# Kernel tuning notes

Hardware: AMD Instinct MI355X
Metric: run time of the kernel (lower is better)

Reference implementation:

```python
import jax, jax.numpy as jnp
import numpy as np

BATCH = 2
SEQ = 2048
D_MODEL = 512
D_STATE = 16
D_CONV = 4
D_INNER = 2 * D_MODEL  # expand=2


def setup_inputs() -> dict:
    key = jax.random.key(0)
    ks = jax.random.split(key, 7)
    s = 0.02
    x = jax.random.normal(ks[0], (BATCH, SEQ, D_MODEL), jnp.float32)
    W_in = jax.random.normal(ks[1], (2 * D_INNER, D_MODEL), jnp.float32) * s
    conv_w = jax.random.normal(ks[2], (D_INNER, 1, D_CONV), jnp.float32) * s  # depthwise kernel
    conv_b = jnp.zeros((D_INNER,), jnp.float32)
    W_x = jax.random.normal(ks[3], (2 * D_STATE, D_INNER), jnp.float32) * s
    W_dt = jax.random.normal(ks[4], (D_INNER, D_INNER), jnp.float32) * s
    b_dt = jnp.zeros((D_INNER,), jnp.float32)
    # A_log init: log of [1..d_state] broadcast over d_inner rows
    A_log = jnp.log(jnp.broadcast_to(jnp.arange(1, D_STATE + 1, dtype=jnp.float32), (D_INNER, D_STATE)))
    D_param = jnp.ones((D_INNER,), jnp.float32)
    W_out = jax.random.normal(ks[5], (D_MODEL, D_INNER), jnp.float32) * s
    return dict(x=x, W_in=W_in, conv_w=conv_w, conv_b=conv_b, W_x=W_x,
                W_dt=W_dt, b_dt=b_dt, A_log=A_log, D_param=D_param, W_out=W_out)


def reference(x, W_in, conv_w, conv_b, W_x, W_dt, b_dt, A_log, D_param, W_out):
    # in_proj, split into x-branch and gate z
    xz = x @ W_in.T                             # [B, L, 2*di]
    xi, z = jnp.split(xz, 2, axis=-1)
    # depthwise causal conv1d (torch pads both sides then slices [:seq_len] == left-pad only)
    h = jnp.transpose(xi, (0, 2, 1))            # [B, di, L]
    h = jax.lax.conv_general_dilated(
        h, conv_w, window_strides=(1,), padding=[(D_CONV - 1, 0)],
        dimension_numbers=('NCH', 'OIH', 'NCH'), feature_group_count=D_INNER)
    h = h + conv_b[None, :, None]
    h = jax.nn.silu(jnp.transpose(h, (0, 2, 1)))  # [B, L, di]

    A = -jnp.exp(A_log)                         # [di, ds]
    x_dbl = h @ W_x.T                           # [B, L, 2*ds]
    _delta_unused, Bmat = jnp.split(x_dbl, 2, axis=-1)  # B (also used as C): [B, L, ds]
    delta = jax.nn.softplus(h @ W_dt.T + b_dt)  # [B, L, di] (overwrites x_proj delta, as in source)

    def step(state, inp):
        d_t, B_t, h_t = inp                     # [B,di], [B,ds], [B,di]
        dA = jnp.exp(d_t[:, :, None] * A)       # [B, di, ds]
        state = dA * state + d_t[:, :, None] * B_t[:, None, :] * h_t[:, :, None]
        y_t = jnp.einsum('bds,bs->bd', state, B_t)  # C == B
        return state, y_t

    init = jnp.zeros((x.shape[0], D_INNER, D_STATE), x.dtype)
    _, ys = jax.lax.scan(step, init,
                         (jnp.swapaxes(delta, 0, 1), jnp.swapaxes(Bmat, 0, 1), jnp.swapaxes(h, 0, 1)))
    y = jnp.swapaxes(ys, 0, 1)                  # [B, L, di]
    y = (y + D_param * h) * jax.nn.silu(z)
    return y @ W_out.T                          # [B, L, d_model]
```

## Files before the change

### kernel.cpp

```cpp
#include <hip/hip_runtime.h>
#include <cstddef>
#include <cstdint>

#define NB 2
#define L_SEQ 2048
#define DM 512
#define DS 16
#define DI 1024
#define NC 64
#define CL (L_SEQ/NC)

typedef __attribute__((ext_vector_type(4))) float f32x4;
typedef __attribute__((ext_vector_type(8))) short bf16x8;

__device__ __forceinline__ float softplus_f(float x) {
  return (x > 20.f) ? x : log1pf(expf(x));
}
__device__ __forceinline__ float silu_f(float x) {
  return x / (1.f + expf(-x));
}
__device__ __forceinline__ ushort f2bf(float f) {
  uint32_t u = __float_as_uint(f);
  return (ushort)((u + 0x7fffu + ((u >> 16) & 1u)) >> 16);
}
__device__ __forceinline__ float bf2f(ushort h) {
  return __uint_as_float(((uint32_t)h) << 16);
}

__device__ __forceinline__ void gload16(const void* g, ushort* lds_wave_base) {
  __builtin_amdgcn_global_load_lds(
      (const __attribute__((address_space(1))) void*)g,
      (__attribute__((address_space(3))) void*)lds_wave_base, 16, 0, 0);
}

template <int N>
__device__ __forceinline__ void wait_vm() {
  if constexpr (N == 0)      asm volatile("s_waitcnt vmcnt(0)" ::: "memory");
  else if constexpr (N == 4) asm volatile("s_waitcnt vmcnt(4)" ::: "memory");
  else if constexpr (N == 6) asm volatile("s_waitcnt vmcnt(6)" ::: "memory");
  else if constexpr (N == 8) asm volatile("s_waitcnt vmcnt(8)" ::: "memory");
}

__global__ __launch_bounds__(256) void split_bf16(
    const float* __restrict__ in, ushort* __restrict__ hi,
    ushort* __restrict__ lo, int n4) {
  int i = blockIdx.x * 256 + threadIdx.x;
  if (i >= n4) return;
  float4 v = ((const float4*)in)[i];
  ushort h0 = f2bf(v.x), h1 = f2bf(v.y), h2 = f2bf(v.z), h3 = f2bf(v.w);
  ((ushort4*)hi)[i] = make_ushort4(h0, h1, h2, h3);
  ((ushort4*)lo)[i] = make_ushort4(
      f2bf(v.x - bf2f(h0)), f2bf(v.y - bf2f(h1)),
      f2bf(v.z - bf2f(h2)), f2bf(v.w - bf2f(h3)));
}

template <int BM, int BN, int ACT>
__global__ __launch_bounds__(256) void gemm_mfma(
    const ushort* __restrict__ Ahi, const ushort* __restrict__ Alo, int lda,
    const ushort* __restrict__ Bhi, const ushort* __restrict__ Blo, int ldb,
    const float* __restrict__ bias, float* __restrict__ C, int ldc, int K) {
  constexpr int AT = BM * 32;
  constexpr int BT = BN * 32;
  constexpr int BUF = 2 * AT + 2 * BT;
  constexpr int MR = BM / 32, NR = BN / 32;
  constexpr int LPS = (BM / 64) * 2 + (BN / 64) * 2;
  __shared__ __align__(16) ushort lds[3 * BUF];

  const int tid = threadIdx.x;
  const int lane = tid & 63;
  const int wave = tid >> 6;
  const int wr = wave >> 1, wc = wave & 1;

  const int nx = gridDim.x;
  const int nwg = nx * gridDim.y;
  int bid = blockIdx.y * nx + blockIdx.x;
  bid = (bid & 7) * (nwg >> 3) + (bid >> 3);
  const int m0 = (bid / nx) * BM;
  const int n0 = (bid % nx) * BN;

  const int r0 = tid >> 2;
  const int kg = (tid & 3) ^ ((r0 >> 1) & 3);
  const size_t aoff0 = (size_t)(m0 + r0) * lda + kg * 8;
  const size_t aoff1 = (size_t)(m0 + r0 + 64) * lda + kg * 8;
  const size_t boff0 = (size_t)(n0 + r0) * ldb + kg * 8;

  const int fr = lane & 15, fq = lane >> 4;
  const int kswz = fq ^ ((fr >> 1) & 3);
  int aoffs[MR], boffs[NR];
#pragma unroll
  for (int m = 0; m < MR; m++) aoffs[m] = (wr * (BM / 2) + m * 16 + fr) * 32 + kswz * 8;
#pragma unroll
  for (int n = 0; n < NR; n++) boffs[n] = (wc * (BN / 2) + n * 16 + fr) * 32 + kswz * 8;

  f32x4 acc[MR][NR];
#pragma unroll
  for (int m = 0; m < MR; m++)
#pragma unroll
    for (int n = 0; n < NR; n++) acc[m][n] = (f32x4){0.f, 0.f, 0.f, 0.f};

  const int nsteps = K >> 5;

#define STAGE(base, kk)                                                     \
  {                                                                         \
    ushort* bp = (base);                                                    \
    gload16(Ahi + aoff0 + (kk), bp + wave * 512);                           \
    if constexpr (BM == 128) gload16(Ahi + aoff1 + (kk), bp + 2048 + wave * 512); \
    gload16(Alo + aoff0 + (kk), bp + AT + wave * 512);                      \
    if constexpr (BM == 128) gload16(Alo + aoff1 + (kk), bp + AT + 2048 + wave * 512); \
    gload16(Bhi + boff0 + (kk), bp + 2 * AT + wave * 512);                  \
    gload16(Blo + boff0 + (kk), bp + 2 * AT + BT + wave * 512);             \
  }

#define COMPUTE(base)                                                          \
  {                                                                            \
    const ushort* cp = (base);                                                 \
    bf16x8 ah[MR], al[MR], bh[NR], bl[NR];                                     \
    _Pragma("unroll")                                                          \
    for (int m = 0; m < MR; m++) ah[m] = *(const bf16x8*)(cp + aoffs[m]);      \
    _Pragma("unroll")                                                          \
    for (int m = 0; m < MR; m++) al[m] = *(const bf16x8*)(cp + AT + aoffs[m]); \
    _Pragma("unroll")                                                          \
    for (int n = 0; n < NR; n++) bh[n] = *(const bf16x8*)(cp + 2 * AT + boffs[n]); \
    _Pragma("unroll")                                                          \
    for (int n = 0; n < NR; n++) bl[n] = *(const bf16x8*)(cp + 2 * AT + BT + boffs[n]); \
    _Pragma("unroll")                                                          \
    for (int m = 0; m < MR; m++)                                               \
      _Pragma("unroll")                                                        \
      for (int n = 0; n < NR; n++)                                             \
        acc[m][n] = __builtin_amdgcn_mfma_f32_16x16x32_bf16(ah[m], bh[n], acc[m][n], 0, 0, 0); \
    _Pragma("unroll")                                                          \
    for (int m = 0; m < MR; m++)                                               \
      _Pragma("unroll")                                                        \
      for (int n = 0; n < NR; n++)                                             \
        acc[m][n] = __builtin_amdgcn_mfma_f32_16x16x32_bf16(al[m], bh[n], acc[m][n], 0, 0, 0); \
    _Pragma("unroll")                                                          \
    for (int m = 0; m < MR; m++)                                               \
      _Pragma("unroll")                                                        \
      for (int n = 0; n < NR; n++)                                             \
        acc[m][n] = __builtin_amdgcn_mfma_f32_16x16x32_bf16(ah[m], bl[n], acc[m][n], 0, 0, 0); \
  }

  STAGE(lds, 0);
  STAGE(lds + BUF, 32);
  int ocur = 0, onext = BUF, ofar = 2 * BUF;
  for (int t = 0; t < nsteps; ++t) {
    if (t == nsteps - 1) wait_vm<0>(); else wait_vm<LPS>();
    __builtin_amdgcn_s_barrier();
    if (t + 2 < nsteps) STAGE(lds + ofar, (t + 2) << 5);
    COMPUTE(lds + ocur);
    int tmp = ocur; ocur = onext; onext = ofar; ofar = tmp;
  }
#undef STAGE
#undef COMPUTE

#pragma unroll
  for (int m = 0; m < MR; m++) {
    const int row = m0 + wr * (BM / 2) + m * 16 + fq * 4;
#pragma unroll
    for (int n = 0; n < NR; n++) {
      const int col = n0 + wc * (BN / 2) + n * 16 + fr;
      float bcol = (ACT == 1) ? bias[col] : 0.f;
#pragma unroll
      for (int j = 0; j < 4; j++) {
        float v = acc[m][n][j];
        if (ACT == 1) v = softplus_f(v + bcol);
        C[(size_t)(row + j) * ldc + col] = v;
      }
    }
  }
}

__global__ __launch_bounds__(256) void conv_silu_kernel(
    const float* __restrict__ xz, const float* __restrict__ conv_w,
    const float* __restrict__ conv_b, float* __restrict__ h,
    ushort* __restrict__ h_hi, ushort* __restrict__ h_lo) {
  const int idx = blockIdx.x * 256 + threadIdx.x;
  const int c = idx & (DI - 1);
  const int r = idx >> 10;
  const int l = r & (L_SEQ - 1);
  const float w0 = conv_w[c * 4 + 0];
  const float w1 = conv_w[c * 4 + 1];
  const float w2 = conv_w[c * 4 + 2];
  const float w3 = conv_w[c * 4 + 3];
  const float* xp = xz + (size_t)r * (2 * DI) + c;
  float acc = conv_b[c];
  if (l >= 3) acc += xp[-3 * 2 * DI] * w0;
  if (l >= 2) acc += xp[-2 * 2 * DI] * w1;
  if (l >= 1) acc += xp[-1 * 2 * DI] * w2;
  acc += xp[0] * w3;
  const float hv = silu_f(acc);
  h[idx] = hv;
  const ushort hh = f2bf(hv);
  h_hi[idx] = hh;
  h_lo[idx] = f2bf(hv - bf2f(hh));
}

__global__ __launch_bounds__(256) void xproj_kernel(
    const float* __restrict__ h, const float* __restrict__ W_x,
    float* __restrict__ Bm) {
  const int idx = blockIdx.x * 256 + threadIdx.x;
  const int s = idx & 15;
  const int r = idx >> 4;
  const float* hp = h + (size_t)r * DI;
  const float* wp = W_x + (size_t)(DS + s) * DI;
  float acc = 0.f;
  for (int k = 0; k < DI; k += 4) {
    float4 hv = *(const float4*)(hp + k);
    float4 wv = *(const float4*)(wp + k);
    acc += hv.x * wv.x + hv.y * wv.y + hv.z * wv.z + hv.w * wv.w;
  }
  Bm[idx] = acc;
}

__global__ __launch_bounds__(256) void scan_phase1(
    const float* __restrict__ delta, const float* __restrict__ h,
    const float* __restrict__ Bm, const float* __restrict__ A_log,
    float* __restrict__ aprod, float* __restrict__ blocal) {
  __shared__ float sB[CL * DS];
  const int tid = threadIdx.x;
  const int bid = blockIdx.x;
  const int cblk = bid & 3;
  const int chunk = (bid >> 2) & (NC - 1);
  const int b = bid >> 8;
  const int c = cblk * 256 + tid;
  const size_t row0 = (size_t)b * L_SEQ + chunk * CL;
  ((float2*)sB)[tid] = ((const float2*)(Bm + row0 * DS))[tid];
  __syncthreads();

  float Acs[DS], state[DS];
#pragma unroll
  for (int s = 0; s < DS; s += 4) {
    float4 al = *(const float4*)(A_log + (size_t)c * DS + s);
    Acs[s + 0] = -__expf(al.x);
    Acs[s + 1] = -__expf(al.y);
    Acs[s + 2] = -__expf(al.z);
    Acs[s + 3] = -__expf(al.w);
    state[s + 0] = 0.f; state[s + 1] = 0.f; state[s + 2] = 0.f; state[s + 3] = 0.f;
  }
  const float* dp = delta + row0 * DI + c;
  const float* hp = h + row0 * DI + c;
  float sdt = 0.f;
  for (int t = 0; t < CL; ++t) {
    const float dt = dp[(size_t)t * DI];
    const float ht = hp[(size_t)t * DI];
    const float dth = dt * ht;
    sdt += dt;
#pragma unroll
    for (int s = 0; s < DS; ++s)
      state[s] = __expf(dt * Acs[s]) * state[s] + dth * sB[t * DS + s];
  }
  const size_t o = (((size_t)b * NC + chunk) * DI + c) * DS;
#pragma unroll
  for (int s = 0; s < DS; s += 4) {
    *(float4*)(aprod + o + s) = make_float4(
        __expf(Acs[s] * sdt), __expf(Acs[s + 1] * sdt),
        __expf(Acs[s + 2] * sdt), __expf(Acs[s + 3] * sdt));
    *(float4*)(blocal + o + s) = make_float4(state[s], state[s + 1], state[s + 2], state[s + 3]);
  }
}

__global__ __launch_bounds__(256) void scan_phase2(
    float* __restrict__ aprod, const float* __restrict__ blocal) {
  const int idx = blockIdx.x * 256 + threadIdx.x;
  const int b = idx >> 14;
  const int cs = idx & 16383;
  float st = 0.f;
  for (int ch = 0; ch < NC; ++ch) {
    const size_t o = (size_t)(b * NC + ch) * (DI * DS) + cs;
    const float a = aprod[o];
    const float bl = blocal[o];
    aprod[o] = st;
    st = a * st + bl;
  }
}

__global__ __launch_bounds__(256) void scan_phase3(
    const float* __restrict__ delta, const float* __restrict__ h,
    const float* __restrict__ Bm, const float* __restrict__ A_log,
    const float* __restrict__ sinit, float* __restrict__ xz,
    const float* __restrict__ Dp) {
  __shared__ float sB[CL * DS];
  const int tid = threadIdx.x;
  const int bid = blockIdx.x;
  const int cblk = bid & 3;
  const int chunk = (bid >> 2) & (NC - 1);
  const int b = bid >> 8;
  const int c = cblk * 256 + tid;
  const size_t row0 = (size_t)b * L_SEQ + chunk * CL;
  ((float2*)sB)[tid] = ((const float2*)(Bm + row0 * DS))[tid];
  __syncthreads();

  float Acs[DS], state[DS];
  const size_t o = (((size_t)b * NC + chunk) * DI + c) * DS;
#pragma unroll
  for (int s = 0; s < DS; s += 4) {
    float4 al = *(const float4*)(A_log + (size_t)c * DS + s);
    Acs[s + 0] = -__expf(al.x);
    Acs[s + 1] = -__expf(al.y);
    Acs[s + 2] = -__expf(al.z);
    Acs[s + 3] = -__expf(al.w);
    float4 sv = *(const float4*)(sinit + o + s);
    state[s + 0] = sv.x; state[s + 1] = sv.y; state[s + 2] = sv.z; state[s + 3] = sv.w;
  }
  const float* dp = delta + row0 * DI + c;
  const float* hp = h + row0 * DI + c;
  const float* zp = xz + row0 * (2 * DI) + DI + c;
  ushort* yrow = (ushort*)(xz + row0 * (2 * DI)) + c;
  const float Dc = Dp[c];
  for (int t = 0; t < CL; ++t) {
    const float dt = dp[(size_t)t * DI];
    const float ht = hp[(size_t)t * DI];
    const float z = zp[(size_t)t * (2 * DI)];
    const float dth = dt * ht;
    float yv = 0.f;
#pragma unroll
    for (int s = 0; s < DS; ++s) {
      const float bt = sB[t * DS + s];
      state[s] = __expf(dt * Acs[s]) * state[s] + dth * bt;
      yv += state[s] * bt;
    }
    const float g = (yv + Dc * ht) * silu_f(z);
    const ushort gh = f2bf(g);
    yrow[(size_t)t * 4096] = gh;
    yrow[(size_t)t * 4096 + 1024] = f2bf(g - bf2f(gh));
  }
}

extern "C" void kernel_launch(void* const* d_in, const int* in_sizes, int n_in,
                              void* d_out, int out_size, void* d_ws, size_t ws_size,
                              hipStream_t stream) {
  const float* x      = (const float*)d_in[0];
  const float* W_in   = (const float*)d_in[1];
  const float* conv_w = (const float*)d_in[2];
  const float* conv_b = (const float*)d_in[3];
  const float* W_x    = (const float*)d_in[4];
  const float* W_dt   = (const float*)d_in[5];
  const float* b_dt   = (const float*)d_in[6];
  const float* A_log  = (const float*)d_in[7];
  const float* D_par  = (const float*)d_in[8];
  const float* W_out  = (const float*)d_in[9];
  float* out = (float*)d_out;

  const int rows = NB * L_SEQ;

  float* xz     = (float*)d_ws;
  float* h      = xz + (size_t)(8u << 20);
  float* delta  = h + (size_t)(4u << 20);
  float* Bm     = delta + (size_t)(4u << 20);
  float* spare  = Bm + (size_t)(64u << 10);
  float* wreg   = spare + (size_t)((3u << 20) / 2);
  ushort* Wdt_hi  = (ushort*)wreg;
  ushort* Wdt_lo  = Wdt_hi + (size_t)(1u << 20);
  ushort* Wout_hi = Wdt_lo + (size_t)(1u << 20);
  ushort* Wout_lo = Wout_hi + (size_t)(512u << 10);
  float* xreg   = wreg + (size_t)((3u << 20) / 2);
  ushort* x_hi  = (ushort*)xreg;
  ushort* x_lo  = x_hi + (size_t)(2u << 20);
  ushort* Win_hi = x_lo + (size_t)(2u << 20);
  ushort* Win_lo = Win_hi + (size_t)(1u << 20);
  ushort* h_hi  = (ushort*)xreg;
  ushort* h_lo  = h_hi + (size_t)(4u << 20);
  float* aprod  = xreg;
  float* blocal = aprod + (size_t)(2u << 20);
  ushort* y_hi  = (ushort*)xz;
  ushort* y_lo  = y_hi + 1024;

  split_bf16<<<2048, 256, 0, stream>>>(x, x_hi, x_lo, rows * DM / 4);
  split_bf16<<<1024, 256, 0, stream>>>(W_in, Win_hi, Win_lo, 2 * DI * DM / 4);
  split_bf16<<<1024, 256, 0, stream>>>(W_dt, Wdt_hi, Wdt_lo, DI * DI / 4);
  split_bf16<<<512, 256, 0, stream>>>(W_out, Wout_hi, Wout_lo, DM * DI / 4);

  gemm_mfma<128, 64, 0><<<dim3(32, 32), 256, 0, stream>>>(
      x_hi, x_lo, DM, Win_hi, Win_lo, DM, nullptr, xz, 2 * DI, DM);
  conv_silu_kernel<<<(rows * DI) / 256, 256, 0, stream>>>(xz, conv_w, conv_b, h, h_hi, h_lo);
  gemm_mfma<128, 64, 1><<<dim3(16, 32), 256, 0, stream>>>(
      h_hi, h_lo, DI, Wdt_hi, Wdt_lo, DI, b_dt, delta, DI, DI);
  xproj_kernel<<<(rows * DS) / 256, 256, 0, stream>>>(h, W_x, Bm);
  scan_phase1<<<NB * NC * (DI / 256), 256, 0, stream>>>(delta, h, Bm, A_log, aprod, blocal);
  scan_phase2<<<(NB * DI * DS) / 256, 256, 0, stream>>>(aprod, blocal);
  scan_phase3<<<NB * NC * (DI / 256), 256, 0, stream>>>(delta, h, Bm, A_log, aprod, xz, D_par);
  gemm_mfma<64, 64, 0><<<dim3(8, 64), 256, 0, stream>>>(
      y_hi, y_lo, 4096, Wout_hi, Wout_lo, DI, nullptr, out, DM, DI);
}
```

Before: 230.6 us.

## Use 8-wave 512-thread GEMM variant for in_proj and dt_proj tiles

Adds a 128x64 split-bf16 MFMA GEMM kernel that runs 8 waves per block instead of 4. Each wave now owns a 32x32 sub-tile and issues 3 global-to-LDS loads per stage instead of 6, with the B hi/lo loads split across the two wave halves. The goal is more waves in flight to hide latency and less staging work per thread, at the cost of more barrier participants and a smaller per-wave MFMA workload. The old kernel is kept only for the 64x64 out-projection, with its BM==128 paths removed.

```diff
diff --git a/kernel.cpp b/kernel.cpp
--- a/kernel.cpp
+++ b/kernel.cpp
@@ -36,9 +36,9 @@
 template <int N>
 __device__ __forceinline__ void wait_vm() {
   if constexpr (N == 0)      asm volatile("s_waitcnt vmcnt(0)" ::: "memory");
+  else if constexpr (N == 3) asm volatile("s_waitcnt vmcnt(3)" ::: "memory");
   else if constexpr (N == 4) asm volatile("s_waitcnt vmcnt(4)" ::: "memory");
   else if constexpr (N == 6) asm volatile("s_waitcnt vmcnt(6)" ::: "memory");
-  else if constexpr (N == 8) asm volatile("s_waitcnt vmcnt(8)" ::: "memory");
 }
 
 __global__ __launch_bounds__(256) void split_bf16(
@@ -54,8 +54,126 @@
       f2bf(v.z - bf2f(h2)), f2bf(v.w - bf2f(h3)));
 }
 
+template <int ACT>
+__global__ __launch_bounds__(512, 4) void gemm_mfma8(
+    const ushort* __restrict__ Ahi, const ushort* __restrict__ Alo, int lda,
+    const ushort* __restrict__ Bhi, const ushort* __restrict__ Blo, int ldb,
+    const float* __restrict__ bias, float* __restrict__ C, int ldc, int K) {
+  constexpr int BM = 128, BN = 64;
+  constexpr int AT = BM * 32;
+  constexpr int BT = BN * 32;
+  constexpr int BUF = 2 * AT + 2 * BT;
+  constexpr int MR = 2, NR = 2;
+  __shared__ __align__(16) ushort lds[3 * BUF];
+
+  const int tid = threadIdx.x;
+  const int lane = tid & 63;
+  const int wave = tid >> 6;
+  const int wr = wave >> 1;
+  const int wc = wave & 1;
+
+  const int nx = gridDim.x;
+  const int nwg = nx * gridDim.y;
+  int bid = blockIdx.y * nx + blockIdx.x;
+  bid = (bid & 7) * (nwg >> 3) + (bid >> 3);
+  const int m0 = (bid / nx) * BM;
+  const int n0 = (bid % nx) * BN;
+
+  const int ra = tid >> 2;
+  const int kga = (tid & 3) ^ ((ra >> 1) & 3);
+  const size_t aoff = (size_t)(m0 + ra) * lda + kga * 8;
+  const int tq = tid & 255;
+  const int rb = tq >> 2;
+  const int kgb = (tq & 3) ^ ((rb >> 1) & 3);
+  const size_t boff = (size_t)(n0 + rb) * ldb + kgb * 8;
+  const ushort* Bsel = (wave < 4) ? Bhi : Blo;
+  const int blds = 2 * AT + ((wave < 4) ? wave * 512 : BT + (wave - 4) * 512);
+
+  const int fr = lane & 15, fq = lane >> 4;
+  const int kswz = fq ^ ((fr >> 1) & 3);
+  int aoffs[MR], boffs[NR];
+#pragma unroll
+  for (int m = 0; m < MR; m++) aoffs[m] = (wr * 32 + m * 16 + fr) * 32 + kswz * 8;
+#pragma unroll
+  for (int n = 0; n < NR; n++) boffs[n] = (wc * 32 + n * 16 + fr) * 32 + kswz * 8;
+
+  f32x4 acc[MR][NR];
+#pragma unroll
+  for (int m = 0; m < MR; m++)
+#pragma unroll
+    for (int n = 0; n < NR; n++) acc[m][n] = (f32x4){0.f, 0.f, 0.f, 0.f};
+
+  const int nsteps = K >> 5;
+
+#define STAGE(base, kk)                                     \
+  {                                                         \
+    ushort* bp = (base);                                    \
+    gload16(Ahi + aoff + (kk), bp + wave * 512);            \
+    gload16(Alo + aoff + (kk), bp + AT + wave * 512);       \
+    gload16(Bsel + boff + (kk), bp + blds);                 \
+  }
+
+#define COMPUTE(base)                                                          \
+  {                                                                            \
+    const ushort* cp = (base);                                                 \
+    bf16x8 ah[MR], al[MR], bh[NR], bl[NR];                                     \
+    _Pragma("unroll")                                                          \
+    for (int m = 0; m < MR; m++) ah[m] = *(const bf16x8*)(cp + aoffs[m]);      \
+    _Pragma("unroll")                                                          \
+    for (int m = 0; m < MR; m++) al[m] = *(const bf16x8*)(cp + AT + aoffs[m]); \
+    _Pragma("unroll")                                                          \
+    for (int n = 0; n < NR; n++) bh[n] = *(const bf16x8*)(cp + 2 * AT + boffs[n]); \
+    _Pragma("unroll")                                                          \
+    for (int n = 0; n < NR; n++) bl[n] = *(const bf16x8*)(cp + 2 * AT + BT + boffs[n]); \
+    _Pragma("unroll")                                                          \
+    for (int m = 0; m < MR; m++)                                               \
+      _Pragma("unroll")                                                        \
+      for (int n = 0; n < NR; n++)                                             \
+        acc[m][n] = __builtin_amdgcn_mfma_f32_16x16x32_bf16(ah[m], bh[n], acc[m][n], 0, 0, 0); \
+    _Pragma("unroll")                                                          \
+    for (int m = 0; m < MR; m++)                                               \
+      _Pragma("unroll")                                                        \
+      for (int n = 0; n < NR; n++)                                             \
+        acc[m][n] = __builtin_amdgcn_mfma_f32_16x16x32_bf16(al[m], bh[n], acc[m][n], 0, 0, 0); \
+    _Pragma("unroll")                                                          \
+    for (int m = 0; m < MR; m++)                                               \
+      _Pragma("unroll")                                                        \
+      for (int n = 0; n < NR; n++)                                             \
+        acc[m][n] = __builtin_amdgcn_mfma_f32_16x16x32_bf16(ah[m], bl[n], acc[m][n], 0, 0, 0); \
+  }
+
+  STAGE(lds, 0);
+  STAGE(lds + BUF, 32);
+  int ocur = 0, onext = BUF, ofar = 2 * BUF;
+  for (int t = 0; t < nsteps; ++t) {
+    if (t == nsteps - 1) wait_vm<0>(); else wait_vm<3>();
+    __builtin_amdgcn_s_barrier();
+    if (t + 2 < nsteps) STAGE(lds + ofar, (t + 2) << 5);
+    COMPUTE(lds + ocur);
+    int tmp = ocur; ocur = onext; onext = ofar; ofar = tmp;
+  }
+#undef STAGE
+#undef COMPUTE
+
+#pragma unroll
+  for (int m = 0; m < MR; m++) {
+    const int row = m0 + wr * 32 + m * 16 + fq * 4;
+#pragma unroll
+    for (int n = 0; n < NR; n++) {
+      const int col = n0 + wc * 32 + n * 16 + fr;
+      float bcol = (ACT == 1) ? bias[col] : 0.f;
+#pragma unroll
+      for (int j = 0; j < 4; j++) {
+        float v = acc[m][n][j];
+        if (ACT == 1) v = softplus_f(v + bcol);
+        C[(size_t)(row + j) * ldc + col] = v;
+      }
+    }
+  }
+}
+
 template <int BM, int BN, int ACT>
-__global__ __launch_bounds__(256) void gemm_mfma(
+__global__ __launch_bounds__(256) void gemm_mfma4(
     const ushort* __restrict__ Ahi, const ushort* __restrict__ Alo, int lda,
     const ushort* __restrict__ Bhi, const ushort* __restrict__ Blo, int ldb,
     const float* __restrict__ bias, float* __restrict__ C, int ldc, int K) {
@@ -81,7 +199,6 @@
   const int r0 = tid >> 2;
   const int kg = (tid & 3) ^ ((r0 >> 1) & 3);
   const size_t aoff0 = (size_t)(m0 + r0) * lda + kg * 8;
-  const size_t aoff1 = (size_t)(m0 + r0 + 64) * lda + kg * 8;
   const size_t boff0 = (size_t)(n0 + r0) * ldb + kg * 8;
 
   const int fr = lane & 15, fq = lane >> 4;
@@ -100,15 +217,13 @@
 
   const int nsteps = K >> 5;
 
-#define STAGE(base, kk)                                                     \
-  {                                                                         \
-    ushort* bp = (base);                                                    \
-    gload16(Ahi + aoff0 + (kk), bp + wave * 512);                           \
-    if constexpr (BM == 128) gload16(Ahi + aoff1 + (kk), bp + 2048 + wave * 512); \
-    gload16(Alo + aoff0 + (kk), bp + AT + wave * 512);                      \
-    if constexpr (BM == 128) gload16(Alo + aoff1 + (kk), bp + AT + 2048 + wave * 512); \
-    gload16(Bhi + boff0 + (kk), bp + 2 * AT + wave * 512);                  \
-    gload16(Blo + boff0 + (kk), bp + 2 * AT + BT + wave * 512);             \
+#define STAGE(base, kk)                                           \
+  {                                                               \
+    ushort* bp = (base);                                          \
+    gload16(Ahi + aoff0 + (kk), bp + wave * 512);                 \
+    gload16(Alo + aoff0 + (kk), bp + AT + wave * 512);            \
+    gload16(Bhi + boff0 + (kk), bp + 2 * AT + wave * 512);        \
+    gload16(Blo + boff0 + (kk), bp + 2 * AT + BT + wave * 512);   \
   }
 
 #define COMPUTE(base)                                                          \
@@ -370,15 +485,15 @@
   split_bf16<<<1024, 256, 0, stream>>>(W_dt, Wdt_hi, Wdt_lo, DI * DI / 4);
   split_bf16<<<512, 256, 0, stream>>>(W_out, Wout_hi, Wout_lo, DM * DI / 4);
 
-  gemm_mfma<128, 64, 0><<<dim3(32, 32), 256, 0, stream>>>(
+  gemm_mfma8<0><<<dim3(32, 32), 512, 0, stream>>>(
       x_hi, x_lo, DM, Win_hi, Win_lo, DM, nullptr, xz, 2 * DI, DM);
   conv_silu_kernel<<<(rows * DI) / 256, 256, 0, stream>>>(xz, conv_w, conv_b, h, h_hi, h_lo);
-  gemm_mfma<128, 64, 1><<<dim3(16, 32), 256, 0, stream>>>(
+  gemm_mfma8<1><<<dim3(16, 32), 512, 0, stream>>>(
       h_hi, h_lo, DI, Wdt_hi, Wdt_lo, DI, b_dt, delta, DI, DI);
   xproj_kernel<<<(rows * DS) / 256, 256, 0, stream>>>(h, W_x, Bm);
   scan_phase1<<<NB * NC * (DI / 256), 256, 0, stream>>>(delta, h, Bm, A_log, aprod, blocal);
   scan_phase2<<<(NB * DI * DS) / 256, 256, 0, stream>>>(aprod, blocal);
   scan_phase3<<<NB * NC * (DI / 256), 256, 0, stream>>>(delta, h, Bm, A_log, aprod, xz, D_par);
-  gemm_mfma<64, 64, 0><<<dim3(8, 64), 256, 0, stream>>>(
+  gemm_mfma4<64, 64, 0><<<dim3(8, 64), 256, 0, stream>>>(
       y_hi, y_lo, 4096, Wout_hi, Wout_lo, DI, nullptr, out, DM, DI);
 }
```

New measurement: 228.3 us. Within noise of the previous version (-1.0%).

## Replace 4-wave GEMM with 2-wave 64-row tiles giving each wave full M strip

Applied to the files above, without the earlier changes.

Replaces the 256-thread GEMM, which split its tile over a 2x2 wave grid, with a 128-thread two-wave kernel. Each wave covers all 64 rows and its own half of the N columns (MR=4, NR up to 4). The in_proj and dt-proj GEMMs now use 64x128 tiles and the out_proj GEMM uses 64x64. The aim is to raise MFMA work per LDS fragment load and to change occupancy and grid shape. The cost is more registers per wave and more global loads per thread per stage, which needs a deeper vmcnt wait.

```diff
diff --git a/kernel.cpp b/kernel.cpp
--- a/kernel.cpp
+++ b/kernel.cpp
@@ -35,10 +35,9 @@
 
 template <int N>
 __device__ __forceinline__ void wait_vm() {
-  if constexpr (N == 0)      asm volatile("s_waitcnt vmcnt(0)" ::: "memory");
-  else if constexpr (N == 4) asm volatile("s_waitcnt vmcnt(4)" ::: "memory");
-  else if constexpr (N == 6) asm volatile("s_waitcnt vmcnt(6)" ::: "memory");
-  else if constexpr (N == 8) asm volatile("s_waitcnt vmcnt(8)" ::: "memory");
+  if constexpr (N == 0)       asm volatile("s_waitcnt vmcnt(0)" ::: "memory");
+  else if constexpr (N == 8)  asm volatile("s_waitcnt vmcnt(8)" ::: "memory");
+  else if constexpr (N == 12) asm volatile("s_waitcnt vmcnt(12)" ::: "memory");
 }
 
 __global__ __launch_bounds__(256) void split_bf16(
@@ -54,22 +53,24 @@
       f2bf(v.z - bf2f(h2)), f2bf(v.w - bf2f(h3)));
 }
 
-template <int BM, int BN, int ACT>
-__global__ __launch_bounds__(256) void gemm_mfma(
+template <int NR, int ACT>
+__global__ __launch_bounds__(128) void gemm_w2(
     const ushort* __restrict__ Ahi, const ushort* __restrict__ Alo, int lda,
     const ushort* __restrict__ Bhi, const ushort* __restrict__ Blo, int ldb,
     const float* __restrict__ bias, float* __restrict__ C, int ldc, int K) {
+  constexpr int BM = 64;
+  constexpr int BN = NR * 32;
+  constexpr int MR = 4;
   constexpr int AT = BM * 32;
   constexpr int BT = BN * 32;
   constexpr int BUF = 2 * AT + 2 * BT;
-  constexpr int MR = BM / 32, NR = BN / 32;
-  constexpr int LPS = (BM / 64) * 2 + (BN / 64) * 2;
+  constexpr int LPS = 4 + 2 * NR;
   __shared__ __align__(16) ushort lds[3 * BUF];
 
   const int tid = threadIdx.x;
   const int lane = tid & 63;
   const int wave = tid >> 6;
-  const int wr = wave >> 1, wc = wave & 1;
+  const int wc = wave;
 
   const int nx = gridDim.x;
   const int nwg = nx * gridDim.y;
@@ -78,19 +79,22 @@
   const int m0 = (bid / nx) * BM;
   const int n0 = (bid % nx) * BN;
 
-  const int r0 = tid >> 2;
-  const int kg = (tid & 3) ^ ((r0 >> 1) & 3);
-  const size_t aoff0 = (size_t)(m0 + r0) * lda + kg * 8;
-  const size_t aoff1 = (size_t)(m0 + r0 + 64) * lda + kg * 8;
-  const size_t boff0 = (size_t)(n0 + r0) * ldb + kg * 8;
+  const int ra = tid >> 2;
+  const int kg = (tid & 3) ^ ((ra >> 1) & 3);
+  const size_t aoff0 = (size_t)(m0 + ra) * lda + kg * 8;
+  const size_t aoff1 = (size_t)(m0 + ra + 32) * lda + kg * 8;
+  size_t boff[NR];
+#pragma unroll
+  for (int i = 0; i < NR; i++)
+    boff[i] = (size_t)(n0 + i * 32 + ra) * ldb + kg * 8;
 
   const int fr = lane & 15, fq = lane >> 4;
   const int kswz = fq ^ ((fr >> 1) & 3);
   int aoffs[MR], boffs[NR];
 #pragma unroll
-  for (int m = 0; m < MR; m++) aoffs[m] = (wr * (BM / 2) + m * 16 + fr) * 32 + kswz * 8;
-#pragma unroll
-  for (int n = 0; n < NR; n++) boffs[n] = (wc * (BN / 2) + n * 16 + fr) * 32 + kswz * 8;
+  for (int m = 0; m < MR; m++) aoffs[m] = (m * 16 + fr) * 32 + kswz * 8;
+#pragma unroll
+  for (int n = 0; n < NR; n++) boffs[n] = (wc * (NR * 16) + n * 16 + fr) * 32 + kswz * 8;
 
   f32x4 acc[MR][NR];
 #pragma unroll
@@ -100,15 +104,18 @@
 
   const int nsteps = K >> 5;
 
-#define STAGE(base, kk)                                                     \
-  {                                                                         \
-    ushort* bp = (base);                                                    \
-    gload16(Ahi + aoff0 + (kk), bp + wave * 512);                           \
-    if constexpr (BM == 128) gload16(Ahi + aoff1 + (kk), bp + 2048 + wave * 512); \
-    gload16(Alo + aoff0 + (kk), bp + AT + wave * 512);                      \
-    if constexpr (BM == 128) gload16(Alo + aoff1 + (kk), bp + AT + 2048 + wave * 512); \
-    gload16(Bhi + boff0 + (kk), bp + 2 * AT + wave * 512);                  \
-    gload16(Blo + boff0 + (kk), bp + 2 * AT + BT + wave * 512);             \
+#define STAGE(base, kk)                                                  \
+  {                                                                      \
+    ushort* bp = (base);                                                 \
+    gload16(Ahi + aoff0 + (kk), bp + wave * 512);                        \
+    gload16(Ahi + aoff1 + (kk), bp + 1024 + wave * 512);                 \
+    gload16(Alo + aoff0 + (kk), bp + AT + wave * 512);                   \
+    gload16(Alo + aoff1 + (kk), bp + AT + 1024 + wave * 512);            \
+    _Pragma("unroll")                                                    \
+    for (int i = 0; i < NR; i++) {                                       \
+      gload16(Bhi + boff[i] + (kk), bp + 2 * AT + i * 1024 + wave * 512);\
+      gload16(Blo + boff[i] + (kk), bp + 2 * AT + BT + i * 1024 + wave * 512);\
+    }                                                                    \
   }
 
 #define COMPUTE(base)                                                          \
@@ -155,10 +162,10 @@
 
 #pragma unroll
   for (int m = 0; m < MR; m++) {
-    const int row = m0 + wr * (BM / 2) + m * 16 + fq * 4;
+    const int row = m0 + m * 16 + fq * 4;
 #pragma unroll
     for (int n = 0; n < NR; n++) {
-      const int col = n0 + wc * (BN / 2) + n * 16 + fr;
+      const int col = n0 + wc * (NR * 16) + n * 16 + fr;
       float bcol = (ACT == 1) ? bias[col] : 0.f;
 #pragma unroll
       for (int j = 0; j < 4; j++) {
@@ -370,15 +377,15 @@
   split_bf16<<<1024, 256, 0, stream>>>(W_dt, Wdt_hi, Wdt_lo, DI * DI / 4);
   split_bf16<<<512, 256, 0, stream>>>(W_out, Wout_hi, Wout_lo, DM * DI / 4);
 
-  gemm_mfma<128, 64, 0><<<dim3(32, 32), 256, 0, stream>>>(
+  gemm_w2<4, 0><<<dim3(16, 64), 128, 0, stream>>>(
       x_hi, x_lo, DM, Win_hi, Win_lo, DM, nullptr, xz, 2 * DI, DM);
   conv_silu_kernel<<<(rows * DI) / 256, 256, 0, stream>>>(xz, conv_w, conv_b, h, h_hi, h_lo);
-  gemm_mfma<128, 64, 1><<<dim3(16, 32), 256, 0, stream>>>(
+  gemm_w2<4, 1><<<dim3(8, 64), 128, 0, stream>>>(
       h_hi, h_lo, DI, Wdt_hi, Wdt_lo, DI, b_dt, delta, DI, DI);
   xproj_kernel<<<(rows * DS) / 256, 256, 0, stream>>>(h, W_x, Bm);
   scan_phase1<<<NB * NC * (DI / 256), 256, 0, stream>>>(delta, h, Bm, A_log, aprod, blocal);
   scan_phase2<<<(NB * DI * DS) / 256, 256, 0, stream>>>(aprod, blocal);
   scan_phase3<<<NB * NC * (DI / 256), 256, 0, stream>>>(delta, h, Bm, A_log, aprod, xz, D_par);
-  gemm_mfma<64, 64, 0><<<dim3(8, 64), 256, 0, stream>>>(
+  gemm_w2<2, 0><<<dim3(8, 64), 128, 0, stream>>>(
       y_hi, y_lo, 4096, Wout_hi, Wout_lo, DI, nullptr, out, DM, DI);
 }
```

After: 263.9 us. 14.4% more time.

## Fuse x_proj B-matrix into delta GEMM and retile GEMMs to BN=128

Applied to the files above, without the earlier changes.

Appends the 16 W_x rows that produce B after W_dt in a combined split-bf16 weight buffer. The delta GEMM then computes both outputs, writing softplus(delta) and Bm from its epilogue, which removes the separate scalar fp32 x_proj kernel. All GEMMs move to BN=128 tiles with 512- or 256-thread blocks and a simpler double-buffered pipeline using __syncthreads, replacing the triple-buffered vmcnt-based one. The delta GEMM wastes part of its last column tile (1152 columns for 1040 used), and the simpler pipeline overlaps loads with compute less.

```diff
diff --git a/kernel.cpp b/kernel.cpp
--- a/kernel.cpp
+++ b/kernel.cpp
@@ -31,14 +31,6 @@
   __builtin_amdgcn_global_load_lds(
       (const __attribute__((address_space(1))) void*)g,
       (__attribute__((address_space(3))) void*)lds_wave_base, 16, 0, 0);
-}
-
-template <int N>
-__device__ __forceinline__ void wait_vm() {
-  if constexpr (N == 0)      asm volatile("s_waitcnt vmcnt(0)" ::: "memory");
-  else if constexpr (N == 4) asm volatile("s_waitcnt vmcnt(4)" ::: "memory");
-  else if constexpr (N == 6) asm volatile("s_waitcnt vmcnt(6)" ::: "memory");
-  else if constexpr (N == 8) asm volatile("s_waitcnt vmcnt(8)" ::: "memory");
 }
 
 __global__ __launch_bounds__(256) void split_bf16(
@@ -54,22 +46,24 @@
       f2bf(v.z - bf2f(h2)), f2bf(v.w - bf2f(h3)));
 }
 
-template <int BM, int BN, int ACT>
-__global__ __launch_bounds__(256) void gemm_mfma(
+template <int BM, int ACT>
+__global__ __launch_bounds__(BM * 4, (BM == 128) ? 4 : 3) void gemm_mfma(
     const ushort* __restrict__ Ahi, const ushort* __restrict__ Alo, int lda,
     const ushort* __restrict__ Bhi, const ushort* __restrict__ Blo, int ldb,
-    const float* __restrict__ bias, float* __restrict__ C, int ldc, int K) {
+    const float* __restrict__ bias, float* __restrict__ C, int ldc,
+    float* __restrict__ Bmout, int K) {
+  constexpr int BN = 128;
   constexpr int AT = BM * 32;
   constexpr int BT = BN * 32;
   constexpr int BUF = 2 * AT + 2 * BT;
-  constexpr int MR = BM / 32, NR = BN / 32;
-  constexpr int LPS = (BM / 64) * 2 + (BN / 64) * 2;
-  __shared__ __align__(16) ushort lds[3 * BUF];
+  constexpr int MR = 4, NR = 2;
+  __shared__ __align__(16) ushort lds[2 * BUF];
 
   const int tid = threadIdx.x;
   const int lane = tid & 63;
   const int wave = tid >> 6;
-  const int wr = wave >> 1, wc = wave & 1;
+  const int wr = wave >> 2;
+  const int wc = wave & 3;
 
   const int nx = gridDim.x;
   const int nwg = nx * gridDim.y;
@@ -78,19 +72,19 @@
   const int m0 = (bid / nx) * BM;
   const int n0 = (bid % nx) * BN;
 
-  const int r0 = tid >> 2;
-  const int kg = (tid & 3) ^ ((r0 >> 1) & 3);
-  const size_t aoff0 = (size_t)(m0 + r0) * lda + kg * 8;
-  const size_t aoff1 = (size_t)(m0 + r0 + 64) * lda + kg * 8;
-  const size_t boff0 = (size_t)(n0 + r0) * ldb + kg * 8;
+  const int ra = tid >> 2;
+  const int kga = (tid & 3) ^ ((ra >> 1) & 3);
+  const size_t aoff  = (size_t)(m0 + ra) * lda + kga * 8;
+  const size_t boff0 = (size_t)(n0 + ra) * ldb + kga * 8;
+  const size_t boff1 = (size_t)(n0 + ra + 64) * ldb + kga * 8;
 
   const int fr = lane & 15, fq = lane >> 4;
   const int kswz = fq ^ ((fr >> 1) & 3);
   int aoffs[MR], boffs[NR];
 #pragma unroll
-  for (int m = 0; m < MR; m++) aoffs[m] = (wr * (BM / 2) + m * 16 + fr) * 32 + kswz * 8;
-#pragma unroll
-  for (int n = 0; n < NR; n++) boffs[n] = (wc * (BN / 2) + n * 16 + fr) * 32 + kswz * 8;
+  for (int m = 0; m < MR; m++) aoffs[m] = (wr * 64 + m * 16 + fr) * 32 + kswz * 8;
+#pragma unroll
+  for (int n = 0; n < NR; n++) boffs[n] = (wc * 32 + n * 16 + fr) * 32 + kswz * 8;
 
   f32x4 acc[MR][NR];
 #pragma unroll
@@ -103,12 +97,14 @@
 #define STAGE(base, kk)                                                     \
   {                                                                         \
     ushort* bp = (base);                                                    \
-    gload16(Ahi + aoff0 + (kk), bp + wave * 512);                           \
-    if constexpr (BM == 128) gload16(Ahi + aoff1 + (kk), bp + 2048 + wave * 512); \
-    gload16(Alo + aoff0 + (kk), bp + AT + wave * 512);                      \
-    if constexpr (BM == 128) gload16(Alo + aoff1 + (kk), bp + AT + 2048 + wave * 512); \
+    gload16(Ahi + aoff + (kk), bp + wave * 512);                            \
+    gload16(Alo + aoff + (kk), bp + AT + wave * 512);                       \
     gload16(Bhi + boff0 + (kk), bp + 2 * AT + wave * 512);                  \
     gload16(Blo + boff0 + (kk), bp + 2 * AT + BT + wave * 512);             \
+    if constexpr (BM == 64) {                                               \
+      gload16(Bhi + boff1 + (kk), bp + 2 * AT + 2048 + wave * 512);         \
+      gload16(Blo + boff1 + (kk), bp + 2 * AT + BT + 2048 + wave * 512);    \
+    }                                                                       \
   }
 
 #define COMPUTE(base)                                                          \
@@ -141,30 +137,36 @@
   }
 
   STAGE(lds, 0);
-  STAGE(lds + BUF, 32);
-  int ocur = 0, onext = BUF, ofar = 2 * BUF;
+  __syncthreads();
   for (int t = 0; t < nsteps; ++t) {
-    if (t == nsteps - 1) wait_vm<0>(); else wait_vm<LPS>();
-    __builtin_amdgcn_s_barrier();
-    if (t + 2 < nsteps) STAGE(lds + ofar, (t + 2) << 5);
-    COMPUTE(lds + ocur);
-    int tmp = ocur; ocur = onext; onext = ofar; ofar = tmp;
+    if (t + 1 < nsteps) STAGE(lds + ((t + 1) & 1) * BUF, (t + 1) << 5);
+    COMPUTE(lds + (t & 1) * BUF);
+    __syncthreads();
   }
 #undef STAGE
 #undef COMPUTE
 
 #pragma unroll
   for (int m = 0; m < MR; m++) {
-    const int row = m0 + wr * (BM / 2) + m * 16 + fq * 4;
+    const int row = m0 + wr * 64 + m * 16 + fq * 4;
 #pragma unroll
     for (int n = 0; n < NR; n++) {
-      const int col = n0 + wc * (BN / 2) + n * 16 + fr;
-      float bcol = (ACT == 1) ? bias[col] : 0.f;
-#pragma unroll
-      for (int j = 0; j < 4; j++) {
-        float v = acc[m][n][j];
-        if (ACT == 1) v = softplus_f(v + bcol);
-        C[(size_t)(row + j) * ldc + col] = v;
+      const int col = n0 + wc * 32 + n * 16 + fr;
+      if (ACT == 1) {
+        if (col < DI) {
+          const float bcol = bias[col];
+#pragma unroll
+          for (int j = 0; j < 4; j++)
+            C[(size_t)(row + j) * ldc + col] = softplus_f(acc[m][n][j] + bcol);
+        } else if (col < DI + DS) {
+#pragma unroll
+          for (int j = 0; j < 4; j++)
+            Bmout[(size_t)(row + j) * DS + (col - DI)] = acc[m][n][j];
+        }
+      } else {
+#pragma unroll
+        for (int j = 0; j < 4; j++)
+          C[(size_t)(row + j) * ldc + col] = acc[m][n][j];
       }
     }
   }
@@ -195,23 +197,6 @@
   h_lo[idx] = f2bf(hv - bf2f(hh));
 }
 
-__global__ __launch_bounds__(256) void xproj_kernel(
-    const float* __restrict__ h, const float* __restrict__ W_x,
-    float* __restrict__ Bm) {
-  const int idx = blockIdx.x * 256 + threadIdx.x;
-  const int s = idx & 15;
-  const int r = idx >> 4;
-  const float* hp = h + (size_t)r * DI;
-  const float* wp = W_x + (size_t)(DS + s) * DI;
-  float acc = 0.f;
-  for (int k = 0; k < DI; k += 4) {
-    float4 hv = *(const float4*)(hp + k);
-    float4 wv = *(const float4*)(wp + k);
-    acc += hv.x * wv.x + hv.y * wv.y + hv.z * wv.z + hv.w * wv.w;
-  }
-  Bm[idx] = acc;
-}
-
 __global__ __launch_bounds__(256) void scan_phase1(
     const float* __restrict__ delta, const float* __restrict__ h,
     const float* __restrict__ Bm, const float* __restrict__ A_log,
@@ -347,13 +332,11 @@
   float* h      = xz + (size_t)(8u << 20);
   float* delta  = h + (size_t)(4u << 20);
   float* Bm     = delta + (size_t)(4u << 20);
-  float* spare  = Bm + (size_t)(64u << 10);
-  float* wreg   = spare + (size_t)((3u << 20) / 2);
-  ushort* Wdt_hi  = (ushort*)wreg;
-  ushort* Wdt_lo  = Wdt_hi + (size_t)(1u << 20);
-  ushort* Wout_hi = Wdt_lo + (size_t)(1u << 20);
+  ushort* W2hi  = (ushort*)(Bm + (size_t)(64u << 10));
+  ushort* W2lo  = W2hi + (size_t)1152 * 1024;
+  ushort* Wout_hi = W2lo + (size_t)1152 * 1024;
   ushort* Wout_lo = Wout_hi + (size_t)(512u << 10);
-  float* xreg   = wreg + (size_t)((3u << 20) / 2);
+  float* xreg   = (float*)(Wout_lo + (size_t)(512u << 10));
   ushort* x_hi  = (ushort*)xreg;
   ushort* x_lo  = x_hi + (size_t)(2u << 20);
   ushort* Win_hi = x_lo + (size_t)(2u << 20);
@@ -367,18 +350,19 @@
 
   split_bf16<<<2048, 256, 0, stream>>>(x, x_hi, x_lo, rows * DM / 4);
   split_bf16<<<1024, 256, 0, stream>>>(W_in, Win_hi, Win_lo, 2 * DI * DM / 4);
-  split_bf16<<<1024, 256, 0, stream>>>(W_dt, Wdt_hi, Wdt_lo, DI * DI / 4);
+  split_bf16<<<1024, 256, 0, stream>>>(W_dt, W2hi, W2lo, DI * DI / 4);
+  split_bf16<<<16, 256, 0, stream>>>(W_x + DS * DI,
+      W2hi + (size_t)DI * DI, W2lo + (size_t)DI * DI, DS * DI / 4);
   split_bf16<<<512, 256, 0, stream>>>(W_out, Wout_hi, Wout_lo, DM * DI / 4);
 
-  gemm_mfma<128, 64, 0><<<dim3(32, 32), 256, 0, stream>>>(
-      x_hi, x_lo, DM, Win_hi, Win_lo, DM, nullptr, xz, 2 * DI, DM);
+  gemm_mfma<128, 0><<<dim3(16, 32), 512, 0, stream>>>(
+      x_hi, x_lo, DM, Win_hi, Win_lo, DM, nullptr, xz, 2 * DI, nullptr, DM);
   conv_silu_kernel<<<(rows * DI) / 256, 256, 0, stream>>>(xz, conv_w, conv_b, h, h_hi, h_lo);
-  gemm_mfma<128, 64, 1><<<dim3(16, 32), 256, 0, stream>>>(
-      h_hi, h_lo, DI, Wdt_hi, Wdt_lo, DI, b_dt, delta, DI, DI);
-  xproj_kernel<<<(rows * DS) / 256, 256, 0, stream>>>(h, W_x, Bm);
+  gemm_mfma<128, 1><<<dim3(9, 32), 512, 0, stream>>>(
+      h_hi, h_lo, DI, W2hi, W2lo, DI, b_dt, delta, DI, Bm, DI);
   scan_phase1<<<NB * NC * (DI / 256), 256, 0, stream>>>(delta, h, Bm, A_log, aprod, blocal);
   scan_phase2<<<(NB * DI * DS) / 256, 256, 0, stream>>>(aprod, blocal);
   scan_phase3<<<NB * NC * (DI / 256), 256, 0, stream>>>(delta, h, Bm, A_log, aprod, xz, D_par);
-  gemm_mfma<64, 64, 0><<<dim3(8, 64), 256, 0, stream>>>(
-      y_hi, y_lo, 4096, Wout_hi, Wout_lo, DI, nullptr, out, DM, DI);
-}
+  gemm_mfma<64, 0><<<dim3(4, 64), 256, 0, stream>>>(
+      y_hi, y_lo, 4096, Wout_hi, Wout_lo, DI, nullptr, out, DM, nullptr, DI);
+}
```

After: 213.6 us. 1.08x faster.
